# Kernel tuning notes

Hardware: AMD Instinct MI355X
Metric: run time of the kernel (lower is better)

The kernel has to match this reference:

```python
import jax, jax.numpy as jnp
import numpy as np

INPUT_SIZE = 2
HIDDEN = 128
OUTPUT = 2
FUTURE = 50


def setup_inputs() -> dict:
    key = jax.random.key(0)
    ks = jax.random.split(key, 7)
    B, T = 4096, 512
    s = 1.0 / np.sqrt(HIDDEN)
    x = jax.random.normal(ks[0], (B, T, INPUT_SIZE), dtype=jnp.float32)
    W_ih = jax.random.uniform(ks[1], (4 * HIDDEN, INPUT_SIZE), minval=-s, maxval=s, dtype=jnp.float32)
    W_hh = jax.random.uniform(ks[2], (4 * HIDDEN, HIDDEN), minval=-s, maxval=s, dtype=jnp.float32)
    b_ih = jax.random.uniform(ks[3], (4 * HIDDEN,), minval=-s, maxval=s, dtype=jnp.float32)
    b_hh = jax.random.uniform(ks[4], (4 * HIDDEN,), minval=-s, maxval=s, dtype=jnp.float32)
    fc_w = jax.random.uniform(ks[5], (OUTPUT, HIDDEN), minval=-s, maxval=s, dtype=jnp.float32)
    fc_b = jax.random.uniform(ks[6], (OUTPUT,), minval=-s, maxval=s, dtype=jnp.float32)
    return {"x": x, "W_ih": W_ih, "W_hh": W_hh, "b_ih": b_ih, "b_hh": b_hh, "fc_w": fc_w, "fc_b": fc_b}


def reference(x, W_ih, W_hh, b_ih, b_hh, fc_w, fc_b):
    B = x.shape[0]

    def cell(h, c, xt):
        # gates: [B, 4H], PyTorch LSTMCell order i, f, g, o
        gates = xt @ W_ih.T + b_ih + h @ W_hh.T + b_hh
        i, f, g, o = jnp.split(gates, 4, axis=-1)
        c_new = jax.nn.sigmoid(f) * c + jax.nn.sigmoid(i) * jnp.tanh(g)
        h_new = jax.nn.sigmoid(o) * jnp.tanh(c_new)
        return h_new, c_new

    h0 = jnp.zeros((B, HIDDEN), dtype=x.dtype)
    c0 = jnp.zeros((B, HIDDEN), dtype=x.dtype)

    def encode_step(carry, xt):
        h, c = carry
        h, c = cell(h, c, xt)
        return (h, c), None

    (h, c), _ = jax.lax.scan(encode_step, (h0, c0), jnp.swapaxes(x, 0, 1))

    def forecast_step(carry, _):
        h, c = carry
        y = h @ fc_w.T + fc_b  # [B, OUTPUT]
        h, c = cell(h, c, y)
        return (h, c), y

    (_, _), ys = jax.lax.scan(forecast_step, (h, c), None, length=FUTURE)
    # ys: [FUTURE, B, OUTPUT] -> torch.cat(outputs, dim=1) -> [B, FUTURE*OUTPUT]
    return jnp.swapaxes(ys, 0, 1).reshape(B, FUTURE * OUTPUT)
```

## Files before the change

kernel.cpp:

```cpp
#include <hip/hip_runtime.h>

#define HIDDEN 128
#define TSTEPS 512
#define NFUT 50
#define BR 16
#define THREADS 512
#define HPITCH 136

typedef __bf16 bf16x8 __attribute__((ext_vector_type(8)));
typedef float floatx4 __attribute__((ext_vector_type(4)));
typedef float f32x2 __attribute__((ext_vector_type(2)));

union B8 { int4 i; bf16x8 v; };

#if defined(__has_builtin)
#  if __has_builtin(__builtin_amdgcn_exp2f)
#    define EXP2F(x) __builtin_amdgcn_exp2f(x)
#  else
#    define EXP2F(x) exp2f(x)
#  endif
#  if __has_builtin(__builtin_amdgcn_rcpf)
#    define RCPF(x) __builtin_amdgcn_rcpf(x)
#  else
#    define RCPF(x) (1.0f / (x))
#  endif
#  if __has_builtin(__builtin_amdgcn_s_setprio)
#    define SETPRIO(p) __builtin_amdgcn_s_setprio(p)
#  else
#    define SETPRIO(p)
#  endif
#else
#  define EXP2F(x) exp2f(x)
#  define RCPF(x) (1.0f / (x))
#  define SETPRIO(p)
#endif

#define L2E  1.4426950408889634f
#define L2E2 2.8853900817779268f

__global__ __launch_bounds__(THREADS, 2)
void lstm_forecast_kernel(const float* __restrict__ x,
                          const float* __restrict__ W_ih,
                          const float* __restrict__ W_hh,
                          const float* __restrict__ b_ih,
                          const float* __restrict__ b_hh,
                          const float* __restrict__ fc_w,
                          const float* __restrict__ fc_b,
                          float* __restrict__ out) {
    __shared__ __align__(16) uint2  xa[TSTEPS * BR];
    __shared__ __align__(16) __bf16 h_lds[2][BR * HPITCH];
    __shared__ __align__(16) float  fcw_lds[2][HIDDEN];

    const int tid  = threadIdx.x;
    const int wave = tid >> 6;
    const int lane = tid & 63;
    const int quad = lane >> 4;
    const int l15  = lane & 15;
    const int rb   = blockIdx.x * BR;

    if (tid < 256) fcw_lds[tid >> 7][tid & 127] = fc_w[tid];

    {
        const int row = tid & 15;
        for (int tb = tid >> 4; tb < TSTEPS; tb += THREADS >> 4) {
            float2 xv = *(const float2*)&x[(size_t)(rb + row) * (2 * TSTEPS) + tb * 2];
            __bf16 x0h = (__bf16)xv.x, x1h = (__bf16)xv.y;
            __bf16 x0r = (__bf16)(xv.x - (float)x0h);
            __bf16 x1r = (__bf16)(xv.y - (float)x1h);
            uint2 d;
            d.x = (unsigned)__builtin_bit_cast(unsigned short, x0h) |
                  ((unsigned)__builtin_bit_cast(unsigned short, x1h) << 16);
            d.y = (unsigned)__builtin_bit_cast(unsigned short, x0r) |
                  ((unsigned)__builtin_bit_cast(unsigned short, x1r) << 16);
            xa[tb * BR + row] = d;
        }
    }
    for (int i = tid; i < BR * HPITCH; i += THREADS) h_lds[0][i] = (__bf16)0.0f;

    bf16x8 bfrag[4][4];
    B8 bfx[4];
    float wih0[4], wih1[4], bsum[4], gs[4];
    const int u = wave * 16 + l15;
    const float fcb0 = fc_b[0], fcb1 = fc_b[1];
#pragma unroll
    for (int g = 0; g < 4; ++g) {
        gs[g] = (g == 2) ? -L2E2 : -L2E;
        const int cg = g * HIDDEN + u;
        wih0[g] = W_ih[cg * 2 + 0];
        wih1[g] = W_ih[cg * 2 + 1];
        bsum[g] = b_ih[cg] + b_hh[cg];
#pragma unroll
        for (int ks = 0; ks < 4; ++ks) {
            const float* wp = W_hh + (size_t)cg * HIDDEN + ks * 32 + quad * 8;
            bf16x8 bb;
#pragma unroll
            for (int j = 0; j < 8; ++j) bb[j] = (__bf16)(gs[g] * wp[j]);
            bfrag[g][ks] = bb;
        }
        B8 t; t.i = make_int4(0, 0, 0, 0);
        if (quad == 0) {
            const float w0s = gs[g] * wih0[g], w1s = gs[g] * wih1[g], bss = gs[g] * bsum[g];
            __bf16 w0h = (__bf16)w0s, w1h = (__bf16)w1s;
            __bf16 w0l = (__bf16)(w0s - (float)w0h);
            __bf16 w1l = (__bf16)(w1s - (float)w1h);
            __bf16 bh  = (__bf16)bss;
            __bf16 bl  = (__bf16)(bss - (float)bh);
            bf16x8 bv = {w0h, w1h, bh, bl, w0h, w1h, w0l, w1l};
            t.v = bv;
        }
        bfx[g] = t;
    }

    const unsigned ones2 = 0x3F803F80u;

    f32x2 cst[2] = {{0.f, 0.f}, {0.f, 0.f}};

    auto ew = [&](floatx4 a0, floatx4 a1, floatx4 a2, floatx4 a3, __bf16* hd) {
#pragma unroll
        for (int p = 0; p < 2; ++p) {
            const f32x2 ap0 = {a0[2*p], a0[2*p+1]};
            const f32x2 ap1 = {a1[2*p], a1[2*p+1]};
            const f32x2 ap2 = {a2[2*p], a2[2*p+1]};
            const f32x2 ap3 = {a3[2*p], a3[2*p+1]};
            f32x2 ea, eb, ec;
            ea.x = EXP2F(ap0.x); ea.y = EXP2F(ap0.y);
            eb.x = EXP2F(ap2.x); eb.y = EXP2F(ap2.y);
            ec.x = EXP2F(ap1.x); ec.y = EXP2F(ap1.y);
            const f32x2 A1 = 1.f + ea, B1 = 1.f + eb, C1 = 1.f + ec;
            const f32x2 P  = A1 * B1;
            const f32x2 PC = P * C1;
            f32x2 R;
            {
                const float I = RCPF(PC.x * PC.y);
                R.x = I * PC.y;
                R.y = I * PC.x;
            }
            const f32x2 sfv = P * R;
            const f32x2 igv = (1.f - eb) * (C1 * R);
            const f32x2 cn  = sfv * cst[p] + igv;
            cst[p] = cn;
            const f32x2 am = -L2E2 * cn;
            f32x2 ed, eo;
            ed.x = EXP2F(fminf(am.x, 29.f));
            ed.y = EXP2F(fminf(am.y, 29.f));
            eo.x = EXP2F(ap3.x); eo.y = EXP2F(ap3.y);
            const f32x2 E = (1.f + ed) * (1.f + eo);
            f32x2 R2;
            {
                const float J = RCPF(E.x * E.y);
                R2.x = J * E.y;
                R2.y = J * E.x;
            }
            const f32x2 hn = (1.f - ed) * R2;
            hd[(quad * 4 + 2*p + 0) * HPITCH + u] = (__bf16)hn.x;
            hd[(quad * 4 + 2*p + 1) * HPITCH + u] = (__bf16)hn.y;
        }
    };

    auto cellE = [&](const __bf16* hs, __bf16* hd, int t) {
        const uint2 xd = xa[t * BR + l15];
        B8 xf; xf.i = make_int4((int)xd.x, (int)ones2, (int)xd.y, (int)xd.x);
        bf16x8 af[4];
#pragma unroll
        for (int ks = 0; ks < 4; ++ks)
            af[ks] = *(const bf16x8*)&hs[l15 * HPITCH + ks * 32 + quad * 8];
        const floatx4 z = {0.f, 0.f, 0.f, 0.f};
        floatx4 acc[4];
        SETPRIO(1);
#pragma unroll
        for (int g = 0; g < 4; ++g)
            acc[g] = __builtin_amdgcn_mfma_f32_16x16x32_bf16(xf.v, bfx[g].v, z, 0, 0, 0);
#pragma unroll
        for (int ks = 0; ks < 4; ++ks)
#pragma unroll
            for (int g = 0; g < 4; ++g)
                acc[g] = __builtin_amdgcn_mfma_f32_16x16x32_bf16(af[ks], bfrag[g][ks], acc[g], 0, 0, 0);
        SETPRIO(0);
        ew(acc[0], acc[1], acc[2], acc[3], hd);
        __syncthreads();
    };

    __syncthreads();

    for (int t = 0; t < TSTEPS; t += 2) {
        cellE(h_lds[0], h_lds[1], t);
        cellE(h_lds[1], h_lds[0], t + 1);
    }

    float bs2[4];
#pragma unroll
    for (int g = 0; g < 4; ++g) {
        bs2[g] = gs[g] * (bsum[g] + wih0[g] * fcb0 + wih1[g] * fcb1);
#pragma unroll
        for (int ks = 0; ks < 4; ++ks) {
            const int k0 = ks * 32 + quad * 8;
            bf16x8 bb = bfrag[g][ks];
#pragma unroll
            for (int j = 0; j < 8; ++j) {
                const float wv = (float)bb[j] + gs[g] * (wih0[g] * fcw_lds[0][k0 + j]
                                                      + wih1[g] * fcw_lds[1][k0 + j]);
                bb[j] = (__bf16)wv;
            }
            bfrag[g][ks] = bb;
        }
    }

    auto cellF = [&](const __bf16* hs, __bf16* hd) {
        bf16x8 af[4];
#pragma unroll
        for (int ks = 0; ks < 4; ++ks)
            af[ks] = *(const bf16x8*)&hs[l15 * HPITCH + ks * 32 + quad * 8];
        floatx4 acc[4];
#pragma unroll
        for (int g = 0; g < 4; ++g)
            acc[g] = (floatx4){bs2[g], bs2[g], bs2[g], bs2[g]};
        SETPRIO(1);
#pragma unroll
        for (int ks = 0; ks < 4; ++ks)
#pragma unroll
            for (int g = 0; g < 4; ++g)
                acc[g] = __builtin_amdgcn_mfma_f32_16x16x32_bf16(af[ks], bfrag[g][ks], acc[g], 0, 0, 0);
        SETPRIO(0);
        ew(acc[0], acc[1], acc[2], acc[3], hd);
        __syncthreads();
    };

    auto emitY = [&](const __bf16* hs, int f) {
        if (wave == 0) {
            const int r = lane & 15, seg = lane >> 4;
            const __bf16* hp = &hs[r * HPITCH + seg * 32];
            float p0 = 0.f, p1 = 0.f;
#pragma unroll
            for (int js = 0; js < 4; ++js) {
                bf16x8 hv = *(const bf16x8*)&hp[js * 8];
                const float4* f0 = (const float4*)&fcw_lds[0][seg * 32 + js * 8];
                const float4* f1 = (const float4*)&fcw_lds[1][seg * 32 + js * 8];
                float4 a0 = f0[0], b0 = f0[1], a1 = f1[0], b1 = f1[1];
                p0 += (float)hv[0]*a0.x + (float)hv[1]*a0.y + (float)hv[2]*a0.z + (float)hv[3]*a0.w
                    + (float)hv[4]*b0.x + (float)hv[5]*b0.y + (float)hv[6]*b0.z + (float)hv[7]*b0.w;
                p1 += (float)hv[0]*a1.x + (float)hv[1]*a1.y + (float)hv[2]*a1.z + (float)hv[3]*a1.w
                    + (float)hv[4]*b1.x + (float)hv[5]*b1.y + (float)hv[6]*b1.z + (float)hv[7]*b1.w;
            }
            p0 += __shfl_xor(p0, 16); p0 += __shfl_xor(p0, 32);
            p1 += __shfl_xor(p1, 16); p1 += __shfl_xor(p1, 32);
            if (seg == 0) {
                float* op = &out[(size_t)(rb + r) * (2 * NFUT) + f * 2];
                op[0] = p0 + fcb0;
                op[1] = p1 + fcb1;
            }
        }
    };

    for (int f = 0; f < NFUT; f += 2) {
        emitY(h_lds[0], f);
        cellF(h_lds[0], h_lds[1]);
        emitY(h_lds[1], f + 1);
        cellF(h_lds[1], h_lds[0]);
    }
}

extern "C" void kernel_launch(void* const* d_in, const int* in_sizes, int n_in,
                              void* d_out, int out_size, void* d_ws, size_t ws_size,
                              hipStream_t stream) {
    const float* x    = (const float*)d_in[0];
    const float* W_ih = (const float*)d_in[1];
    const float* W_hh = (const float*)d_in[2];
    const float* b_ih = (const float*)d_in[3];
    const float* b_hh = (const float*)d_in[4];
    const float* fc_w = (const float*)d_in[5];
    const float* fc_b = (const float*)d_in[6];
    float* out = (float*)d_out;

    const int B = in_sizes[0] / (TSTEPS * 2);
    const int grid = B / BR;
    lstm_forecast_kernel<<<grid, THREADS, 0, stream>>>(x, W_ih, W_hh, b_ih, b_hh, fc_w, fc_b, out);
}
```

Measured before the change: 495.6 us.

## Halve waves per block, give each wave two unit tiles with interleaved MFMA/elementwise

Cuts the block to 4 waves, each owning 32 hidden units (two 16-unit tiles) instead of 16. It also swaps MFMA operand order so each lane holds consecutive hidden units, allowing packed 8-byte h stores. The second tile's MFMAs are interleaved with the first tile's elementwise gate math to overlap matrix and vector work within a wave, and s_setprio is dropped. The cost is double the register weight fragments per thread and fewer waves to hide latency.

Measured after the change: 567.9 us. +14.6%, slower.

```diff
diff --git a/kernel.cpp b/kernel.cpp
--- a/kernel.cpp
+++ b/kernel.cpp
@@ -4,7 +4,7 @@
 #define TSTEPS 512
 #define NFUT 50
 #define BR 16
-#define THREADS 512
+#define THREADS 256
 #define HPITCH 136
 
 typedef __bf16 bf16x8 __attribute__((ext_vector_type(8)));
@@ -24,21 +24,15 @@
 #  else
 #    define RCPF(x) (1.0f / (x))
 #  endif
-#  if __has_builtin(__builtin_amdgcn_s_setprio)
-#    define SETPRIO(p) __builtin_amdgcn_s_setprio(p)
-#  else
-#    define SETPRIO(p)
-#  endif
 #else
 #  define EXP2F(x) exp2f(x)
 #  define RCPF(x) (1.0f / (x))
-#  define SETPRIO(p)
 #endif
 
 #define L2E  1.4426950408889634f
 #define L2E2 2.8853900817779268f
 
-__global__ __launch_bounds__(THREADS, 2)
+__global__ __launch_bounds__(THREADS, 1)
 void lstm_forecast_kernel(const float* __restrict__ x,
                           const float* __restrict__ W_ih,
                           const float* __restrict__ W_hh,
@@ -77,84 +71,85 @@
     }
     for (int i = tid; i < BR * HPITCH; i += THREADS) h_lds[0][i] = (__bf16)0.0f;
 
-    bf16x8 bfrag[4][4];
-    B8 bfx[4];
-    float wih0[4], wih1[4], bsum[4], gs[4];
-    const int u = wave * 16 + l15;
+    bf16x8 bfrag[2][4][4];
+    B8 bfx[2][4];
+    float gs[4];
     const float fcb0 = fc_b[0], fcb1 = fc_b[1];
 #pragma unroll
-    for (int g = 0; g < 4; ++g) {
-        gs[g] = (g == 2) ? -L2E2 : -L2E;
-        const int cg = g * HIDDEN + u;
-        wih0[g] = W_ih[cg * 2 + 0];
-        wih1[g] = W_ih[cg * 2 + 1];
-        bsum[g] = b_ih[cg] + b_hh[cg];
-#pragma unroll
-        for (int ks = 0; ks < 4; ++ks) {
-            const float* wp = W_hh + (size_t)cg * HIDDEN + ks * 32 + quad * 8;
-            bf16x8 bb;
-#pragma unroll
-            for (int j = 0; j < 8; ++j) bb[j] = (__bf16)(gs[g] * wp[j]);
-            bfrag[g][ks] = bb;
-        }
-        B8 t; t.i = make_int4(0, 0, 0, 0);
-        if (quad == 0) {
-            const float w0s = gs[g] * wih0[g], w1s = gs[g] * wih1[g], bss = gs[g] * bsum[g];
-            __bf16 w0h = (__bf16)w0s, w1h = (__bf16)w1s;
-            __bf16 w0l = (__bf16)(w0s - (float)w0h);
-            __bf16 w1l = (__bf16)(w1s - (float)w1h);
-            __bf16 bh  = (__bf16)bss;
-            __bf16 bl  = (__bf16)(bss - (float)bh);
-            bf16x8 bv = {w0h, w1h, bh, bl, w0h, w1h, w0l, w1l};
-            t.v = bv;
-        }
-        bfx[g] = t;
+    for (int g = 0; g < 4; ++g) gs[g] = (g == 2) ? -L2E2 : -L2E;
+#pragma unroll
+    for (int s = 0; s < 2; ++s) {
+        const int ub = wave * 32 + s * 16 + l15;
+#pragma unroll
+        for (int g = 0; g < 4; ++g) {
+            const int cg = g * HIDDEN + ub;
+            const float w0 = W_ih[cg * 2 + 0];
+            const float w1 = W_ih[cg * 2 + 1];
+            const float bs = b_ih[cg] + b_hh[cg];
+#pragma unroll
+            for (int ks = 0; ks < 4; ++ks) {
+                const float* wp = W_hh + (size_t)cg * HIDDEN + ks * 32 + quad * 8;
+                bf16x8 bb;
+#pragma unroll
+                for (int j = 0; j < 8; ++j) bb[j] = (__bf16)(gs[g] * wp[j]);
+                bfrag[s][g][ks] = bb;
+            }
+            B8 t; t.i = make_int4(0, 0, 0, 0);
+            if (quad == 0) {
+                const float w0s = gs[g] * w0, w1s = gs[g] * w1, bss = gs[g] * bs;
+                __bf16 w0h = (__bf16)w0s, w1h = (__bf16)w1s;
+                __bf16 w0l = (__bf16)(w0s - (float)w0h);
+                __bf16 w1l = (__bf16)(w1s - (float)w1h);
+                __bf16 bh  = (__bf16)bss;
+                __bf16 bl  = (__bf16)(bss - (float)bh);
+                bf16x8 bv = {w0h, w1h, bh, bl, w0h, w1h, w0l, w1l};
+                t.v = bv;
+            }
+            bfx[s][g] = t;
+        }
     }
 
     const unsigned ones2 = 0x3F803F80u;
-
-    f32x2 cst[2] = {{0.f, 0.f}, {0.f, 0.f}};
-
-    auto ew = [&](floatx4 a0, floatx4 a1, floatx4 a2, floatx4 a3, __bf16* hd) {
-#pragma unroll
-        for (int p = 0; p < 2; ++p) {
-            const f32x2 ap0 = {a0[2*p], a0[2*p+1]};
-            const f32x2 ap1 = {a1[2*p], a1[2*p+1]};
-            const f32x2 ap2 = {a2[2*p], a2[2*p+1]};
-            const f32x2 ap3 = {a3[2*p], a3[2*p+1]};
-            f32x2 ea, eb, ec;
-            ea.x = EXP2F(ap0.x); ea.y = EXP2F(ap0.y);
-            eb.x = EXP2F(ap2.x); eb.y = EXP2F(ap2.y);
-            ec.x = EXP2F(ap1.x); ec.y = EXP2F(ap1.y);
-            const f32x2 A1 = 1.f + ea, B1 = 1.f + eb, C1 = 1.f + ec;
-            const f32x2 P  = A1 * B1;
-            const f32x2 PC = P * C1;
-            f32x2 R;
-            {
-                const float I = RCPF(PC.x * PC.y);
-                R.x = I * PC.y;
-                R.y = I * PC.x;
-            }
-            const f32x2 sfv = P * R;
-            const f32x2 igv = (1.f - eb) * (C1 * R);
-            const f32x2 cn  = sfv * cst[p] + igv;
-            cst[p] = cn;
-            const f32x2 am = -L2E2 * cn;
-            f32x2 ed, eo;
-            ed.x = EXP2F(fminf(am.x, 29.f));
-            ed.y = EXP2F(fminf(am.y, 29.f));
-            eo.x = EXP2F(ap3.x); eo.y = EXP2F(ap3.y);
-            const f32x2 E = (1.f + ed) * (1.f + eo);
-            f32x2 R2;
-            {
-                const float J = RCPF(E.x * E.y);
-                R2.x = J * E.y;
-                R2.y = J * E.x;
-            }
-            const f32x2 hn = (1.f - ed) * R2;
-            hd[(quad * 4 + 2*p + 0) * HPITCH + u] = (__bf16)hn.x;
-            hd[(quad * 4 + 2*p + 1) * HPITCH + u] = (__bf16)hn.y;
-        }
+    const int hrow = l15 * HPITCH;
+    const int c0   = wave * 32 + quad * 4;
+
+    f32x2 cst[2][2] = {{{0.f, 0.f}, {0.f, 0.f}}, {{0.f, 0.f}, {0.f, 0.f}}};
+
+    auto mk = [](float a, float b) { f32x2 r; r.x = a; r.y = b; return r; };
+
+    auto ewPair = [&](f32x2 ap0, f32x2 ap1, f32x2 ap2, f32x2 ap3, f32x2& c) -> unsigned {
+        f32x2 ea, eb, ec;
+        ea.x = EXP2F(ap0.x); ea.y = EXP2F(ap0.y);
+        eb.x = EXP2F(ap2.x); eb.y = EXP2F(ap2.y);
+        ec.x = EXP2F(ap1.x); ec.y = EXP2F(ap1.y);
+        const f32x2 A1 = 1.f + ea, B1 = 1.f + eb, C1 = 1.f + ec;
+        const f32x2 P  = A1 * B1;
+        const f32x2 PC = P * C1;
+        f32x2 R;
+        {
+            const float I = RCPF(PC.x * PC.y);
+            R.x = I * PC.y;
+            R.y = I * PC.x;
+        }
+        const f32x2 sfv = P * R;
+        const f32x2 igv = (1.f - eb) * (C1 * R);
+        const f32x2 cn  = sfv * c + igv;
+        c = cn;
+        const f32x2 am = -L2E2 * cn;
+        f32x2 ed, eo;
+        ed.x = EXP2F(fminf(am.x, 29.f));
+        ed.y = EXP2F(fminf(am.y, 29.f));
+        eo.x = EXP2F(ap3.x); eo.y = EXP2F(ap3.y);
+        const f32x2 E = (1.f + ed) * (1.f + eo);
+        f32x2 R2;
+        {
+            const float J = RCPF(E.x * E.y);
+            R2.x = J * E.y;
+            R2.y = J * E.x;
+        }
+        const f32x2 hn = (1.f - ed) * R2;
+        return (unsigned)__builtin_bit_cast(unsigned short, (__bf16)hn.x)
+             | ((unsigned)__builtin_bit_cast(unsigned short, (__bf16)hn.y) << 16);
     };
 
     auto cellE = [&](const __bf16* hs, __bf16* hd, int t) {
@@ -163,20 +158,40 @@
         bf16x8 af[4];
 #pragma unroll
         for (int ks = 0; ks < 4; ++ks)
-            af[ks] = *(const bf16x8*)&hs[l15 * HPITCH + ks * 32 + quad * 8];
+            af[ks] = *(const bf16x8*)&hs[hrow + ks * 32 + quad * 8];
         const floatx4 z = {0.f, 0.f, 0.f, 0.f};
-        floatx4 acc[4];
-        SETPRIO(1);
+        floatx4 a0[4], a1[4];
 #pragma unroll
         for (int g = 0; g < 4; ++g)
-            acc[g] = __builtin_amdgcn_mfma_f32_16x16x32_bf16(xf.v, bfx[g].v, z, 0, 0, 0);
+            a0[g] = __builtin_amdgcn_mfma_f32_16x16x32_bf16(bfx[0][g].v, xf.v, z, 0, 0, 0);
 #pragma unroll
         for (int ks = 0; ks < 4; ++ks)
 #pragma unroll
             for (int g = 0; g < 4; ++g)
-                acc[g] = __builtin_amdgcn_mfma_f32_16x16x32_bf16(af[ks], bfrag[g][ks], acc[g], 0, 0, 0);
-        SETPRIO(0);
-        ew(acc[0], acc[1], acc[2], acc[3], hd);
+                a0[g] = __builtin_amdgcn_mfma_f32_16x16x32_bf16(bfrag[0][g][ks], af[ks], a0[g], 0, 0, 0);
+#pragma unroll
+        for (int g = 0; g < 4; ++g)
+            a1[g] = __builtin_amdgcn_mfma_f32_16x16x32_bf16(bfx[1][g].v, xf.v, z, 0, 0, 0);
+#pragma unroll
+        for (int ks = 0; ks < 2; ++ks)
+#pragma unroll
+            for (int g = 0; g < 4; ++g)
+                a1[g] = __builtin_amdgcn_mfma_f32_16x16x32_bf16(bfrag[1][g][ks], af[ks], a1[g], 0, 0, 0);
+        const unsigned lo0 = ewPair(mk(a0[0][0], a0[0][1]), mk(a0[1][0], a0[1][1]),
+                                    mk(a0[2][0], a0[2][1]), mk(a0[3][0], a0[3][1]), cst[0][0]);
+#pragma unroll
+        for (int ks = 2; ks < 4; ++ks)
+#pragma unroll
+            for (int g = 0; g < 4; ++g)
+                a1[g] = __builtin_amdgcn_mfma_f32_16x16x32_bf16(bfrag[1][g][ks], af[ks], a1[g], 0, 0, 0);
+        const unsigned hi0 = ewPair(mk(a0[0][2], a0[0][3]), mk(a0[1][2], a0[1][3]),
+                                    mk(a0[2][2], a0[2][3]), mk(a0[3][2], a0[3][3]), cst[0][1]);
+        { uint2 w; w.x = lo0; w.y = hi0; *(uint2*)&hd[hrow + c0] = w; }
+        const unsigned lo1 = ewPair(mk(a1[0][0], a1[0][1]), mk(a1[1][0], a1[1][1]),
+                                    mk(a1[2][0], a1[2][1]), mk(a1[3][0], a1[3][1]), cst[1][0]);
+        const unsigned hi1 = ewPair(mk(a1[0][2], a1[0][3]), mk(a1[1][2], a1[1][3]),
+                                    mk(a1[2][2], a1[2][3]), mk(a1[3][2], a1[3][3]), cst[1][1]);
+        { uint2 w; w.x = lo1; w.y = hi1; *(uint2*)&hd[hrow + c0 + 16] = w; }
         __syncthreads();
     };
 
@@ -187,21 +202,33 @@
         cellE(h_lds[1], h_lds[0], t + 1);
     }
 
-    float bs2[4];
-#pragma unroll
-    for (int g = 0; g < 4; ++g) {
-        bs2[g] = gs[g] * (bsum[g] + wih0[g] * fcb0 + wih1[g] * fcb1);
-#pragma unroll
-        for (int ks = 0; ks < 4; ++ks) {
-            const int k0 = ks * 32 + quad * 8;
-            bf16x8 bb = bfrag[g][ks];
-#pragma unroll
-            for (int j = 0; j < 8; ++j) {
-                const float wv = (float)bb[j] + gs[g] * (wih0[g] * fcw_lds[0][k0 + j]
-                                                      + wih1[g] * fcw_lds[1][k0 + j]);
-                bb[j] = (__bf16)wv;
-            }
-            bfrag[g][ks] = bb;
+    floatx4 bs2v[2][4];
+#pragma unroll
+    for (int s = 0; s < 2; ++s) {
+        const int ub = wave * 32 + s * 16 + l15;
+#pragma unroll
+        for (int g = 0; g < 4; ++g) {
+            const int cg = g * HIDDEN + ub;
+            const float wi0 = W_ih[cg * 2 + 0];
+            const float wi1 = W_ih[cg * 2 + 1];
+            const float bs  = b_ih[cg] + b_hh[cg];
+            const float b2  = gs[g] * (bs + wi0 * fcb0 + wi1 * fcb1);
+#pragma unroll
+            for (int ks = 0; ks < 4; ++ks) {
+                const int k0 = ks * 32 + quad * 8;
+                bf16x8 bb = bfrag[s][g][ks];
+#pragma unroll
+                for (int j = 0; j < 8; ++j) {
+                    const float wv = (float)bb[j] + gs[g] * (wi0 * fcw_lds[0][k0 + j]
+                                                          + wi1 * fcw_lds[1][k0 + j]);
+                    bb[j] = (__bf16)wv;
+                }
+                bfrag[s][g][ks] = bb;
+            }
+            floatx4 v;
+#pragma unroll
+            for (int r = 0; r < 4; ++r) v[r] = __shfl(b2, quad * 4 + r);
+            bs2v[s][g] = v;
         }
     }
 
@@ -209,19 +236,37 @@
         bf16x8 af[4];
 #pragma unroll
         for (int ks = 0; ks < 4; ++ks)
-            af[ks] = *(const bf16x8*)&hs[l15 * HPITCH + ks * 32 + quad * 8];
-        floatx4 acc[4];
-#pragma unroll
-        for (int g = 0; g < 4; ++g)
-            acc[g] = (floatx4){bs2[g], bs2[g], bs2[g], bs2[g]};
-        SETPRIO(1);
+            af[ks] = *(const bf16x8*)&hs[hrow + ks * 32 + quad * 8];
+        floatx4 a0[4], a1[4];
+#pragma unroll
+        for (int g = 0; g < 4; ++g) a0[g] = bs2v[0][g];
 #pragma unroll
         for (int ks = 0; ks < 4; ++ks)
 #pragma unroll
             for (int g = 0; g < 4; ++g)
-                acc[g] = __builtin_amdgcn_mfma_f32_16x16x32_bf16(af[ks], bfrag[g][ks], acc[g], 0, 0, 0);
-        SETPRIO(0);
-        ew(acc[0], acc[1], acc[2], acc[3], hd);
+                a0[g] = __builtin_amdgcn_mfma_f32_16x16x32_bf16(bfrag[0][g][ks], af[ks], a0[g], 0, 0, 0);
+#pragma unroll
+        for (int g = 0; g < 4; ++g) a1[g] = bs2v[1][g];
+#pragma unroll
+        for (int ks = 0; ks < 2; ++ks)
+#pragma unroll
+            for (int g = 0; g < 4; ++g)
+                a1[g] = __builtin_amdgcn_mfma_f32_16x16x32_bf16(bfrag[1][g][ks], af[ks], a1[g], 0, 0, 0);
+        const unsigned lo0 = ewPair(mk(a0[0][0], a0[0][1]), mk(a0[1][0], a0[1][1]),
+                                    mk(a0[2][0], a0[2][1]), mk(a0[3][0], a0[3][1]), cst[0][0]);
+#pragma unroll
+        for (int ks = 2; ks < 4; ++ks)
+#pragma unroll
+            for (int g = 0; g < 4; ++g)
+                a1[g] = __builtin_amdgcn_mfma_f32_16x16x32_bf16(bfrag[1][g][ks], af[ks], a1[g], 0, 0, 0);
+        const unsigned hi0 = ewPair(mk(a0[0][2], a0[0][3]), mk(a0[1][2], a0[1][3]),
+                                    mk(a0[2][2], a0[2][3]), mk(a0[3][2], a0[3][3]), cst[0][1]);
+        { uint2 w; w.x = lo0; w.y = hi0; *(uint2*)&hd[hrow + c0] = w; }
+        const unsigned lo1 = ewPair(mk(a1[0][0], a1[0][1]), mk(a1[1][0], a1[1][1]),
+                                    mk(a1[2][0], a1[2][1]), mk(a1[3][0], a1[3][1]), cst[1][0]);
+        const unsigned hi1 = ewPair(mk(a1[0][2], a1[0][3]), mk(a1[1][2], a1[1][3]),
+                                    mk(a1[2][2], a1[2][3]), mk(a1[3][2], a1[3][3]), cst[1][1]);
+        { uint2 w; w.x = lo1; w.y = hi1; *(uint2*)&hd[hrow + c0 + 16] = w; }
         __syncthreads();
     };
 
```

## Transpose MFMA operands, fold input projection into FP32 accumulator init, interleave gate exps

Applied to the files above, without the earlier changes.

Swaps the MFMA operand order so each lane owns four consecutive hidden units for one batch row. That lets the new h values go out as a single packed 8-byte LDS store instead of four scattered bf16 stores. The input projection and bias are now computed in fp32 as the accumulator's initial value, replacing the extra bf16 hi/lo MFMA per gate, so x is stored raw in LDS. Gates are computed one at a time with their exp2 right after each MFMA chain, so transcendental work overlaps the later matrix ops. The setprio hints are removed, and the vector FMA work per step grows.

New measurement: 520.8 us. 1.05x slower.

```diff
diff --git a/kernel.cpp b/kernel.cpp
--- a/kernel.cpp
+++ b/kernel.cpp
@@ -10,8 +10,6 @@
 typedef __bf16 bf16x8 __attribute__((ext_vector_type(8)));
 typedef float floatx4 __attribute__((ext_vector_type(4)));
 typedef float f32x2 __attribute__((ext_vector_type(2)));
-
-union B8 { int4 i; bf16x8 v; };
 
 #if defined(__has_builtin)
 #  if __has_builtin(__builtin_amdgcn_exp2f)
@@ -24,15 +22,9 @@
 #  else
 #    define RCPF(x) (1.0f / (x))
 #  endif
-#  if __has_builtin(__builtin_amdgcn_s_setprio)
-#    define SETPRIO(p) __builtin_amdgcn_s_setprio(p)
-#  else
-#    define SETPRIO(p)
-#  endif
 #else
 #  define EXP2F(x) exp2f(x)
 #  define RCPF(x) (1.0f / (x))
-#  define SETPRIO(p)
 #endif
 
 #define L2E  1.4426950408889634f
@@ -47,7 +39,7 @@
                           const float* __restrict__ fc_w,
                           const float* __restrict__ fc_b,
                           float* __restrict__ out) {
-    __shared__ __align__(16) uint2  xa[TSTEPS * BR];
+    __shared__ __align__(16) float2 xa[TSTEPS * BR];
     __shared__ __align__(16) __bf16 h_lds[2][BR * HPITCH];
     __shared__ __align__(16) float  fcw_lds[2][HIDDEN];
 
@@ -62,122 +54,120 @@
 
     {
         const int row = tid & 15;
-        for (int tb = tid >> 4; tb < TSTEPS; tb += THREADS >> 4) {
-            float2 xv = *(const float2*)&x[(size_t)(rb + row) * (2 * TSTEPS) + tb * 2];
-            __bf16 x0h = (__bf16)xv.x, x1h = (__bf16)xv.y;
-            __bf16 x0r = (__bf16)(xv.x - (float)x0h);
-            __bf16 x1r = (__bf16)(xv.y - (float)x1h);
-            uint2 d;
-            d.x = (unsigned)__builtin_bit_cast(unsigned short, x0h) |
-                  ((unsigned)__builtin_bit_cast(unsigned short, x1h) << 16);
-            d.y = (unsigned)__builtin_bit_cast(unsigned short, x0r) |
-                  ((unsigned)__builtin_bit_cast(unsigned short, x1r) << 16);
-            xa[tb * BR + row] = d;
-        }
+        for (int tb = tid >> 4; tb < TSTEPS; tb += THREADS >> 4)
+            xa[tb * BR + row] = *(const float2*)&x[(size_t)(rb + row) * (2 * TSTEPS) + tb * 2];
     }
     for (int i = tid; i < BR * HPITCH; i += THREADS) h_lds[0][i] = (__bf16)0.0f;
 
     bf16x8 bfrag[4][4];
-    B8 bfx[4];
-    float wih0[4], wih1[4], bsum[4], gs[4];
-    const int u = wave * 16 + l15;
+    floatx4 w0c[4], w1c[4], bc[4];
+    floatx4 beff[4];
+    float gs[4];
     const float fcb0 = fc_b[0], fcb1 = fc_b[1];
 #pragma unroll
+    for (int g = 0; g < 4; ++g) gs[g] = (g == 2) ? -L2E2 : -L2E;
+    const int ub    = wave * 16 + l15;
+    const int cbase = wave * 16 + quad * 4;
+#pragma unroll
     for (int g = 0; g < 4; ++g) {
-        gs[g] = (g == 2) ? -L2E2 : -L2E;
-        const int cg = g * HIDDEN + u;
-        wih0[g] = W_ih[cg * 2 + 0];
-        wih1[g] = W_ih[cg * 2 + 1];
-        bsum[g] = b_ih[cg] + b_hh[cg];
 #pragma unroll
         for (int ks = 0; ks < 4; ++ks) {
-            const float* wp = W_hh + (size_t)cg * HIDDEN + ks * 32 + quad * 8;
+            const float* wp = W_hh + (size_t)(g * HIDDEN + ub) * HIDDEN + ks * 32 + quad * 8;
             bf16x8 bb;
 #pragma unroll
             for (int j = 0; j < 8; ++j) bb[j] = (__bf16)(gs[g] * wp[j]);
             bfrag[g][ks] = bb;
         }
-        B8 t; t.i = make_int4(0, 0, 0, 0);
-        if (quad == 0) {
-            const float w0s = gs[g] * wih0[g], w1s = gs[g] * wih1[g], bss = gs[g] * bsum[g];
-            __bf16 w0h = (__bf16)w0s, w1h = (__bf16)w1s;
-            __bf16 w0l = (__bf16)(w0s - (float)w0h);
-            __bf16 w1l = (__bf16)(w1s - (float)w1h);
-            __bf16 bh  = (__bf16)bss;
-            __bf16 bl  = (__bf16)(bss - (float)bh);
-            bf16x8 bv = {w0h, w1h, bh, bl, w0h, w1h, w0l, w1l};
-            t.v = bv;
-        }
-        bfx[g] = t;
-    }
-
-    const unsigned ones2 = 0x3F803F80u;
-
+        floatx4 v0, v1, vb;
+#pragma unroll
+        for (int r = 0; r < 4; ++r) {
+            const int cg = g * HIDDEN + cbase + r;
+            v0[r] = gs[g] * W_ih[cg * 2 + 0];
+            v1[r] = gs[g] * W_ih[cg * 2 + 1];
+            vb[r] = gs[g] * (b_ih[cg] + b_hh[cg]);
+        }
+        w0c[g] = v0; w1c[g] = v1; bc[g] = vb;
+    }
+
+    const int hrow = l15 * HPITCH;
     f32x2 cst[2] = {{0.f, 0.f}, {0.f, 0.f}};
 
-    auto ew = [&](floatx4 a0, floatx4 a1, floatx4 a2, floatx4 a3, __bf16* hd) {
+    auto pk2 = [](f32x2 hn) -> unsigned {
+        return (unsigned)__builtin_bit_cast(unsigned short, (__bf16)hn.x)
+             | ((unsigned)__builtin_bit_cast(unsigned short, (__bf16)hn.y) << 16);
+    };
+
+    auto cellCore = [&](const __bf16* hs, __bf16* hd,
+                        floatx4 a0, floatx4 a1, floatx4 a2, floatx4 a3) {
+        bf16x8 af[4];
+#pragma unroll
+        for (int ks = 0; ks < 4; ++ks)
+            af[ks] = *(const bf16x8*)&hs[hrow + ks * 32 + quad * 8];
+#pragma unroll
+        for (int ks = 0; ks < 4; ++ks)
+            a0 = __builtin_amdgcn_mfma_f32_16x16x32_bf16(bfrag[0][ks], af[ks], a0, 0, 0, 0);
+        floatx4 ea;
+#pragma unroll
+        for (int r = 0; r < 4; ++r) ea[r] = EXP2F(a0[r]);
+#pragma unroll
+        for (int ks = 0; ks < 4; ++ks)
+            a1 = __builtin_amdgcn_mfma_f32_16x16x32_bf16(bfrag[1][ks], af[ks], a1, 0, 0, 0);
+        floatx4 ec;
+#pragma unroll
+        for (int r = 0; r < 4; ++r) ec[r] = EXP2F(a1[r]);
+#pragma unroll
+        for (int ks = 0; ks < 4; ++ks)
+            a2 = __builtin_amdgcn_mfma_f32_16x16x32_bf16(bfrag[2][ks], af[ks], a2, 0, 0, 0);
+        floatx4 eb;
+#pragma unroll
+        for (int r = 0; r < 4; ++r) eb[r] = EXP2F(a2[r]);
+        f32x2 edp[2];
 #pragma unroll
         for (int p = 0; p < 2; ++p) {
-            const f32x2 ap0 = {a0[2*p], a0[2*p+1]};
-            const f32x2 ap1 = {a1[2*p], a1[2*p+1]};
-            const f32x2 ap2 = {a2[2*p], a2[2*p+1]};
-            const f32x2 ap3 = {a3[2*p], a3[2*p+1]};
-            f32x2 ea, eb, ec;
-            ea.x = EXP2F(ap0.x); ea.y = EXP2F(ap0.y);
-            eb.x = EXP2F(ap2.x); eb.y = EXP2F(ap2.y);
-            ec.x = EXP2F(ap1.x); ec.y = EXP2F(ap1.y);
-            const f32x2 A1 = 1.f + ea, B1 = 1.f + eb, C1 = 1.f + ec;
+            const f32x2 eap = {ea[2 * p], ea[2 * p + 1]};
+            const f32x2 ebp = {eb[2 * p], eb[2 * p + 1]};
+            const f32x2 ecp = {ec[2 * p], ec[2 * p + 1]};
+            const f32x2 A1 = 1.f + eap, B1 = 1.f + ebp, C1 = 1.f + ecp;
             const f32x2 P  = A1 * B1;
             const f32x2 PC = P * C1;
             f32x2 R;
-            {
-                const float I = RCPF(PC.x * PC.y);
-                R.x = I * PC.y;
-                R.y = I * PC.x;
-            }
+            { const float I = RCPF(PC.x * PC.y); R.x = I * PC.y; R.y = I * PC.x; }
             const f32x2 sfv = P * R;
-            const f32x2 igv = (1.f - eb) * (C1 * R);
+            const f32x2 igv = (1.f - ebp) * (C1 * R);
             const f32x2 cn  = sfv * cst[p] + igv;
             cst[p] = cn;
             const f32x2 am = -L2E2 * cn;
-            f32x2 ed, eo;
-            ed.x = EXP2F(fminf(am.x, 29.f));
-            ed.y = EXP2F(fminf(am.y, 29.f));
-            eo.x = EXP2F(ap3.x); eo.y = EXP2F(ap3.y);
-            const f32x2 E = (1.f + ed) * (1.f + eo);
+            edp[p].x = EXP2F(fminf(am.x, 29.f));
+            edp[p].y = EXP2F(fminf(am.y, 29.f));
+        }
+#pragma unroll
+        for (int ks = 0; ks < 4; ++ks)
+            a3 = __builtin_amdgcn_mfma_f32_16x16x32_bf16(bfrag[3][ks], af[ks], a3, 0, 0, 0);
+        floatx4 eo;
+#pragma unroll
+        for (int r = 0; r < 4; ++r) eo[r] = EXP2F(a3[r]);
+        unsigned wArr[2];
+#pragma unroll
+        for (int p = 0; p < 2; ++p) {
+            const f32x2 eop = {eo[2 * p], eo[2 * p + 1]};
+            const f32x2 E = (1.f + edp[p]) * (1.f + eop);
             f32x2 R2;
-            {
-                const float J = RCPF(E.x * E.y);
-                R2.x = J * E.y;
-                R2.y = J * E.x;
-            }
-            const f32x2 hn = (1.f - ed) * R2;
-            hd[(quad * 4 + 2*p + 0) * HPITCH + u] = (__bf16)hn.x;
-            hd[(quad * 4 + 2*p + 1) * HPITCH + u] = (__bf16)hn.y;
-        }
+            { const float J = RCPF(E.x * E.y); R2.x = J * E.y; R2.y = J * E.x; }
+            const f32x2 hn = (1.f - edp[p]) * R2;
+            wArr[p] = pk2(hn);
+        }
+        uint2 wv; wv.x = wArr[0]; wv.y = wArr[1];
+        *(uint2*)&hd[hrow + cbase] = wv;
+        __syncthreads();
     };
 
     auto cellE = [&](const __bf16* hs, __bf16* hd, int t) {
-        const uint2 xd = xa[t * BR + l15];
-        B8 xf; xf.i = make_int4((int)xd.x, (int)ones2, (int)xd.y, (int)xd.x);
-        bf16x8 af[4];
-#pragma unroll
-        for (int ks = 0; ks < 4; ++ks)
-            af[ks] = *(const bf16x8*)&hs[l15 * HPITCH + ks * 32 + quad * 8];
-        const floatx4 z = {0.f, 0.f, 0.f, 0.f};
-        floatx4 acc[4];
-        SETPRIO(1);
-#pragma unroll
-        for (int g = 0; g < 4; ++g)
-            acc[g] = __builtin_amdgcn_mfma_f32_16x16x32_bf16(xf.v, bfx[g].v, z, 0, 0, 0);
-#pragma unroll
-        for (int ks = 0; ks < 4; ++ks)
-#pragma unroll
-            for (int g = 0; g < 4; ++g)
-                acc[g] = __builtin_amdgcn_mfma_f32_16x16x32_bf16(af[ks], bfrag[g][ks], acc[g], 0, 0, 0);
-        SETPRIO(0);
-        ew(acc[0], acc[1], acc[2], acc[3], hd);
-        __syncthreads();
+        const float2 xv = xa[t * BR + l15];
+        floatx4 a0 = bc[0] + w0c[0] * xv.x + w1c[0] * xv.y;
+        floatx4 a1 = bc[1] + w0c[1] * xv.x + w1c[1] * xv.y;
+        floatx4 a2 = bc[2] + w0c[2] * xv.x + w1c[2] * xv.y;
+        floatx4 a3 = bc[3] + w0c[3] * xv.x + w1c[3] * xv.y;
+        cellCore(hs, hd, a0, a1, a2, a3);
     };
 
     __syncthreads();
@@ -187,42 +177,26 @@
         cellE(h_lds[1], h_lds[0], t + 1);
     }
 
-    float bs2[4];
 #pragma unroll
     for (int g = 0; g < 4; ++g) {
-        bs2[g] = gs[g] * (bsum[g] + wih0[g] * fcb0 + wih1[g] * fcb1);
+        beff[g] = bc[g] + w0c[g] * fcb0 + w1c[g] * fcb1;
+        const int cg2 = g * HIDDEN + ub;
+        const float wi0 = W_ih[cg2 * 2 + 0];
+        const float wi1 = W_ih[cg2 * 2 + 1];
 #pragma unroll
         for (int ks = 0; ks < 4; ++ks) {
             const int k0 = ks * 32 + quad * 8;
             bf16x8 bb = bfrag[g][ks];
 #pragma unroll
-            for (int j = 0; j < 8; ++j) {
-                const float wv = (float)bb[j] + gs[g] * (wih0[g] * fcw_lds[0][k0 + j]
-                                                      + wih1[g] * fcw_lds[1][k0 + j]);
-                bb[j] = (__bf16)wv;
-            }
+            for (int j = 0; j < 8; ++j)
+                bb[j] = (__bf16)((float)bb[j] + gs[g] * (wi0 * fcw_lds[0][k0 + j]
+                                                       + wi1 * fcw_lds[1][k0 + j]));
             bfrag[g][ks] = bb;
         }
     }
 
     auto cellF = [&](const __bf16* hs, __bf16* hd) {
-        bf16x8 af[4];
-#pragma unroll
-        for (int ks = 0; ks < 4; ++ks)
-            af[ks] = *(const bf16x8*)&hs[l15 * HPITCH + ks * 32 + quad * 8];
-        floatx4 acc[4];
-#pragma unroll
-        for (int g = 0; g < 4; ++g)
-            acc[g] = (floatx4){bs2[g], bs2[g], bs2[g], bs2[g]};
-        SETPRIO(1);
-#pragma unroll
-        for (int ks = 0; ks < 4; ++ks)
-#pragma unroll
-            for (int g = 0; g < 4; ++g)
-                acc[g] = __builtin_amdgcn_mfma_f32_16x16x32_bf16(af[ks], bfrag[g][ks], acc[g], 0, 0, 0);
-        SETPRIO(0);
-        ew(acc[0], acc[1], acc[2], acc[3], hd);
-        __syncthreads();
+        cellCore(hs, hd, beff[0], beff[1], beff[2], beff[3]);
     };
 
     auto emitY = [&](const __bf16* hs, int f) {
```

## Transpose MFMA operands for vectorized h stores and prefetch next x input

Applied to the files above, without the earlier changes.

Swaps the A/B operands of the MFMA so each lane's accumulator holds four consecutive hidden units of one batch row. The new hidden state can then be written to LDS as one packed 8-byte store instead of four scattered 2-byte stores. The next timestep's x value is loaded before the elementwise tail to hide LDS latency, and all exp2 calls are batched up front. Bias is now per-row in the forecast phase, which costs extra registers.

Measured after the change: 477.6 us. 1.04x faster.

```diff
diff --git a/kernel.cpp b/kernel.cpp
--- a/kernel.cpp
+++ b/kernel.cpp
@@ -79,16 +79,17 @@
 
     bf16x8 bfrag[4][4];
     B8 bfx[4];
-    float wih0[4], wih1[4], bsum[4], gs[4];
-    const int u = wave * 16 + l15;
+    float gs[4];
     const float fcb0 = fc_b[0], fcb1 = fc_b[1];
+    const int ub    = wave * 16 + l15;
+    const int cbase = wave * 16 + quad * 4;
 #pragma unroll
     for (int g = 0; g < 4; ++g) {
         gs[g] = (g == 2) ? -L2E2 : -L2E;
-        const int cg = g * HIDDEN + u;
-        wih0[g] = W_ih[cg * 2 + 0];
-        wih1[g] = W_ih[cg * 2 + 1];
-        bsum[g] = b_ih[cg] + b_hh[cg];
+        const int cg = g * HIDDEN + ub;
+        const float w0 = W_ih[cg * 2 + 0];
+        const float w1 = W_ih[cg * 2 + 1];
+        const float bs = b_ih[cg] + b_hh[cg];
 #pragma unroll
         for (int ks = 0; ks < 4; ++ks) {
             const float* wp = W_hh + (size_t)cg * HIDDEN + ks * 32 + quad * 8;
@@ -99,7 +100,7 @@
         }
         B8 t; t.i = make_int4(0, 0, 0, 0);
         if (quad == 0) {
-            const float w0s = gs[g] * wih0[g], w1s = gs[g] * wih1[g], bss = gs[g] * bsum[g];
+            const float w0s = gs[g] * w0, w1s = gs[g] * w1, bss = gs[g] * bs;
             __bf16 w0h = (__bf16)w0s, w1h = (__bf16)w1s;
             __bf16 w0l = (__bf16)(w0s - (float)w0h);
             __bf16 w1l = (__bf16)(w1s - (float)w1h);
@@ -112,116 +113,129 @@
     }
 
     const unsigned ones2 = 0x3F803F80u;
-
+    const int hrow = l15 * HPITCH;
     f32x2 cst[2] = {{0.f, 0.f}, {0.f, 0.f}};
 
-    auto ew = [&](floatx4 a0, floatx4 a1, floatx4 a2, floatx4 a3, __bf16* hd) {
+    auto pk2 = [](f32x2 hn) -> unsigned {
+        return (unsigned)__builtin_bit_cast(unsigned short, (__bf16)hn.x)
+             | ((unsigned)__builtin_bit_cast(unsigned short, (__bf16)hn.y) << 16);
+    };
+
+    auto ewTail = [&](floatx4 a0, floatx4 a1, floatx4 a2, floatx4 a3, __bf16* hd) {
+        floatx4 ea, ec, eb, eo;
+#pragma unroll
+        for (int r = 0; r < 4; ++r) ea[r] = EXP2F(a0[r]);
+#pragma unroll
+        for (int r = 0; r < 4; ++r) ec[r] = EXP2F(a1[r]);
+#pragma unroll
+        for (int r = 0; r < 4; ++r) eb[r] = EXP2F(a2[r]);
+#pragma unroll
+        for (int r = 0; r < 4; ++r) eo[r] = EXP2F(a3[r]);
+        unsigned wArr[2];
 #pragma unroll
         for (int p = 0; p < 2; ++p) {
-            const f32x2 ap0 = {a0[2*p], a0[2*p+1]};
-            const f32x2 ap1 = {a1[2*p], a1[2*p+1]};
-            const f32x2 ap2 = {a2[2*p], a2[2*p+1]};
-            const f32x2 ap3 = {a3[2*p], a3[2*p+1]};
-            f32x2 ea, eb, ec;
-            ea.x = EXP2F(ap0.x); ea.y = EXP2F(ap0.y);
-            eb.x = EXP2F(ap2.x); eb.y = EXP2F(ap2.y);
-            ec.x = EXP2F(ap1.x); ec.y = EXP2F(ap1.y);
-            const f32x2 A1 = 1.f + ea, B1 = 1.f + eb, C1 = 1.f + ec;
+            const f32x2 eap = {ea[2 * p], ea[2 * p + 1]};
+            const f32x2 ebp = {eb[2 * p], eb[2 * p + 1]};
+            const f32x2 ecp = {ec[2 * p], ec[2 * p + 1]};
+            const f32x2 eop = {eo[2 * p], eo[2 * p + 1]};
+            const f32x2 A1 = 1.f + eap, B1 = 1.f + ebp, C1 = 1.f + ecp;
             const f32x2 P  = A1 * B1;
             const f32x2 PC = P * C1;
             f32x2 R;
-            {
-                const float I = RCPF(PC.x * PC.y);
-                R.x = I * PC.y;
-                R.y = I * PC.x;
-            }
+            { const float I = RCPF(PC.x * PC.y); R.x = I * PC.y; R.y = I * PC.x; }
             const f32x2 sfv = P * R;
-            const f32x2 igv = (1.f - eb) * (C1 * R);
+            const f32x2 igv = (1.f - ebp) * (C1 * R);
             const f32x2 cn  = sfv * cst[p] + igv;
             cst[p] = cn;
             const f32x2 am = -L2E2 * cn;
-            f32x2 ed, eo;
+            f32x2 ed;
             ed.x = EXP2F(fminf(am.x, 29.f));
             ed.y = EXP2F(fminf(am.y, 29.f));
-            eo.x = EXP2F(ap3.x); eo.y = EXP2F(ap3.y);
-            const f32x2 E = (1.f + ed) * (1.f + eo);
+            const f32x2 E = (1.f + ed) * (1.f + eop);
             f32x2 R2;
-            {
-                const float J = RCPF(E.x * E.y);
-                R2.x = J * E.y;
-                R2.y = J * E.x;
-            }
+            { const float J = RCPF(E.x * E.y); R2.x = J * E.y; R2.y = J * E.x; }
             const f32x2 hn = (1.f - ed) * R2;
-            hd[(quad * 4 + 2*p + 0) * HPITCH + u] = (__bf16)hn.x;
-            hd[(quad * 4 + 2*p + 1) * HPITCH + u] = (__bf16)hn.y;
-        }
-    };
-
-    auto cellE = [&](const __bf16* hs, __bf16* hd, int t) {
-        const uint2 xd = xa[t * BR + l15];
+            wArr[p] = pk2(hn);
+        }
+        uint2 wv; wv.x = wArr[0]; wv.y = wArr[1];
+        *(uint2*)&hd[hrow + cbase] = wv;
+    };
+
+    auto cellE = [&](const __bf16* hs, __bf16* hd, uint2 xd, int tn) -> uint2 {
         B8 xf; xf.i = make_int4((int)xd.x, (int)ones2, (int)xd.y, (int)xd.x);
         bf16x8 af[4];
 #pragma unroll
         for (int ks = 0; ks < 4; ++ks)
-            af[ks] = *(const bf16x8*)&hs[l15 * HPITCH + ks * 32 + quad * 8];
+            af[ks] = *(const bf16x8*)&hs[hrow + ks * 32 + quad * 8];
         const floatx4 z = {0.f, 0.f, 0.f, 0.f};
         floatx4 acc[4];
         SETPRIO(1);
 #pragma unroll
         for (int g = 0; g < 4; ++g)
-            acc[g] = __builtin_amdgcn_mfma_f32_16x16x32_bf16(xf.v, bfx[g].v, z, 0, 0, 0);
+            acc[g] = __builtin_amdgcn_mfma_f32_16x16x32_bf16(bfx[g].v, xf.v, z, 0, 0, 0);
 #pragma unroll
         for (int ks = 0; ks < 4; ++ks)
 #pragma unroll
             for (int g = 0; g < 4; ++g)
-                acc[g] = __builtin_amdgcn_mfma_f32_16x16x32_bf16(af[ks], bfrag[g][ks], acc[g], 0, 0, 0);
+                acc[g] = __builtin_amdgcn_mfma_f32_16x16x32_bf16(bfrag[g][ks], af[ks], acc[g], 0, 0, 0);
         SETPRIO(0);
-        ew(acc[0], acc[1], acc[2], acc[3], hd);
+        const int ts = (tn < TSTEPS) ? tn : 0;
+        const uint2 xn = xa[ts * BR + l15];
+        ewTail(acc[0], acc[1], acc[2], acc[3], hd);
         __syncthreads();
+        return xn;
     };
 
     __syncthreads();
 
+    uint2 xd = xa[l15];
     for (int t = 0; t < TSTEPS; t += 2) {
-        cellE(h_lds[0], h_lds[1], t);
-        cellE(h_lds[1], h_lds[0], t + 1);
-    }
-
-    float bs2[4];
+        xd = cellE(h_lds[0], h_lds[1], xd, t + 1);
+        xd = cellE(h_lds[1], h_lds[0], xd, t + 2);
+    }
+
+    floatx4 beff[4];
 #pragma unroll
     for (int g = 0; g < 4; ++g) {
-        bs2[g] = gs[g] * (bsum[g] + wih0[g] * fcb0 + wih1[g] * fcb1);
+        const int cgA = g * HIDDEN + ub;
+        const float wi0 = W_ih[cgA * 2 + 0];
+        const float wi1 = W_ih[cgA * 2 + 1];
 #pragma unroll
         for (int ks = 0; ks < 4; ++ks) {
             const int k0 = ks * 32 + quad * 8;
             bf16x8 bb = bfrag[g][ks];
 #pragma unroll
-            for (int j = 0; j < 8; ++j) {
-                const float wv = (float)bb[j] + gs[g] * (wih0[g] * fcw_lds[0][k0 + j]
-                                                      + wih1[g] * fcw_lds[1][k0 + j]);
-                bb[j] = (__bf16)wv;
-            }
+            for (int j = 0; j < 8; ++j)
+                bb[j] = (__bf16)((float)bb[j] + gs[g] * (wi0 * fcw_lds[0][k0 + j]
+                                                       + wi1 * fcw_lds[1][k0 + j]));
             bfrag[g][ks] = bb;
         }
+        floatx4 v;
+#pragma unroll
+        for (int r = 0; r < 4; ++r) {
+            const int cg = g * HIDDEN + cbase + r;
+            v[r] = gs[g] * (b_ih[cg] + b_hh[cg]
+                          + W_ih[cg * 2 + 0] * fcb0 + W_ih[cg * 2 + 1] * fcb1);
+        }
+        beff[g] = v;
     }
 
     auto cellF = [&](const __bf16* hs, __bf16* hd) {
         bf16x8 af[4];
 #pragma unroll
         for (int ks = 0; ks < 4; ++ks)
-            af[ks] = *(const bf16x8*)&hs[l15 * HPITCH + ks * 32 + quad * 8];
+            af[ks] = *(const bf16x8*)&hs[hrow + ks * 32 + quad * 8];
         floatx4 acc[4];
 #pragma unroll
-        for (int g = 0; g < 4; ++g)
-            acc[g] = (floatx4){bs2[g], bs2[g], bs2[g], bs2[g]};
+        for (int g = 0; g < 4; ++g) acc[g] = beff[g];
         SETPRIO(1);
 #pragma unroll
         for (int ks = 0; ks < 4; ++ks)
 #pragma unroll
             for (int g = 0; g < 4; ++g)
-                acc[g] = __builtin_amdgcn_mfma_f32_16x16x32_bf16(af[ks], bfrag[g][ks], acc[g], 0, 0, 0);
+                acc[g] = __builtin_amdgcn_mfma_f32_16x16x32_bf16(bfrag[g][ks], af[ks], acc[g], 0, 0, 0);
         SETPRIO(0);
-        ew(acc[0], acc[1], acc[2], acc[3], hd);
+        ewTail(acc[0], acc[1], acc[2], acc[3], hd);
         __syncthreads();
     };
 
```
